# Performance work log

Measured on AMD Instinct MI355X. Metric: run time of the kernel, lower is better.

## Reference

```python
import jax, jax.numpy as jnp
import numpy as np
from jax import lax

N, D, K = 8192, 1024, 80
M = 2048            # pre-NMS candidate budget (jit-static stand-in for nonzero())
TOPK = 100
IMG_H, IMG_W = 800.0, 1216.0
BW = (10.0, 10.0, 5.0, 5.0)            # Box2BoxTransform weights
SCALE_CLAMP = float(np.log(1000.0 / 16.0))
SCORE_T, NMS_T = 0.05, 0.5
MAX_COORD = max(IMG_H, IMG_W) + 1.0    # class offset for batched NMS


def setup_inputs() -> dict:
    key = jax.random.key(0)
    ks = jax.random.split(key, 5)
    x = jax.random.normal(ks[0], (N, D), jnp.float32)
    cls_w = jax.random.normal(ks[1], (D, K + 1), jnp.float32) * 0.1
    cls_b = jnp.zeros((K + 1,), jnp.float32)
    bbox_w = jax.random.normal(ks[2], (D, K * 4), jnp.float32) * 0.001
    bbox_b = jnp.zeros((K * 4,), jnp.float32)
    xy = jax.random.uniform(ks[3], (N, 2)) * jnp.array([IMG_W * 0.8, IMG_H * 0.8])
    wh = jax.random.uniform(ks[4], (N, 2)) * jnp.array([IMG_W * 0.2, IMG_H * 0.2]) + 8.0
    proposals = jnp.concatenate([xy, xy + wh], axis=1).astype(jnp.float32)  # [N,4] xyxy
    return {"x": x, "cls_w": cls_w, "cls_b": cls_b,
            "bbox_w": bbox_w, "bbox_b": bbox_b, "proposals": proposals}


def _apply_deltas(deltas, boxes):
    # deltas [N,K,4], boxes [N,4] xyxy -> decoded [N,K,4]
    w = boxes[:, 2] - boxes[:, 0]
    h = boxes[:, 3] - boxes[:, 1]
    cx = boxes[:, 0] + 0.5 * w
    cy = boxes[:, 1] + 0.5 * h
    dx = deltas[..., 0] / BW[0]
    dy = deltas[..., 1] / BW[1]
    dw = jnp.minimum(deltas[..., 2] / BW[2], SCALE_CLAMP)
    dh = jnp.minimum(deltas[..., 3] / BW[3], SCALE_CLAMP)
    pcx = dx * w[:, None] + cx[:, None]
    pcy = dy * h[:, None] + cy[:, None]
    pw = jnp.exp(dw) * w[:, None]
    ph = jnp.exp(dh) * h[:, None]
    return jnp.stack([pcx - 0.5 * pw, pcy - 0.5 * ph,
                      pcx + 0.5 * pw, pcy + 0.5 * ph], axis=-1)


def _clip(b):
    x1 = jnp.clip(b[..., 0], 0.0, IMG_W)
    y1 = jnp.clip(b[..., 1], 0.0, IMG_H)
    x2 = jnp.clip(b[..., 2], 0.0, IMG_W)
    y2 = jnp.clip(b[..., 3], 0.0, IMG_H)
    return jnp.stack([x1, y1, x2, y2], axis=-1)


def _pairwise_iou(b):  # [M,4] -> [M,M]
    x1 = jnp.maximum(b[:, None, 0], b[None, :, 0])
    y1 = jnp.maximum(b[:, None, 1], b[None, :, 1])
    x2 = jnp.minimum(b[:, None, 2], b[None, :, 2])
    y2 = jnp.minimum(b[:, None, 3], b[None, :, 3])
    inter = jnp.maximum(x2 - x1, 0.0) * jnp.maximum(y2 - y1, 0.0)
    area = (b[:, 2] - b[:, 0]) * (b[:, 3] - b[:, 1])
    union = area[:, None] + area[None, :] - inter
    return inter / jnp.maximum(union, 1e-9)


def _pipeline(x, cls_w, cls_b, bbox_w, bbox_b, proposals):
    probs = jax.nn.softmax(x @ cls_w + cls_b, axis=-1)[:, :K]   # drop bg col
    deltas = (x @ bbox_w + bbox_b).reshape(N, K, 4)
    boxes = _clip(_apply_deltas(deltas, proposals))             # [N,K,4]

    flat = probs.reshape(-1)                                    # [N*K]
    cand = jnp.where(flat > SCORE_T, flat, -1.0)
    top_scores, top_idx = lax.top_k(cand, M)                    # sorted desc
    prop_idx = top_idx // K
    cls_idx = top_idx % K
    cand_boxes = boxes[prop_idx, cls_idx]                       # [M,4]
    valid = top_scores > SCORE_T

    # batched NMS via per-class coordinate offsets
    off = cls_idx.astype(cand_boxes.dtype)[:, None] * MAX_COORD
    iou = _pairwise_iou(cand_boxes + off)
    idxs = jnp.arange(M)

    def body(i, sup):
        alive = jnp.logical_and(~sup[i], valid[i])
        return sup | (alive & (iou[i] > NMS_T) & (idxs > i))

    sup = lax.fori_loop(0, M, body, jnp.zeros((M,), bool))
    keep = valid & ~sup

    kept_scores = jnp.where(keep, top_scores, -1.0)
    fscores, fidx = lax.top_k(kept_scores, TOPK)
    fboxes = cand_boxes[fidx]
    fcls = cls_idx[fidx]
    fvalid = keep[fidx]
    return fboxes, fscores, fcls, fvalid


def reference(x, cls_w, cls_b, bbox_w, bbox_b, proposals):
    return _pipeline(x, cls_w, cls_b, bbox_w, bbox_b, proposals)
```

## Files before the change

### kernel.cpp

```cpp
#include <hip/hip_runtime.h>
#include <math.h>

typedef unsigned long long u64;
typedef unsigned int u32;

#define N_ROWS 8192
#define DIM 1024
#define KCLS 80
#define KC1 81
#define MCAND 2048
#define TOPK_ 100
#define CMAX 65536
#define ECAP 4096
#define ROWS_CAP 4096
#define EROWS 3
#define EKS 4
#define EKL (DIM / EKS)
#define FRPB 8
#define NSPLIT 4
#define NBINS 8192
#define BIN_BASE 125440
#define LCAP 1024
#define SCORE_T 0.05
#define NMS_T 0.5f
#define MAX_COORD_F 1217.0f
#define SCALE_CLAMP_F 4.135166556742356f
#define IMG_W_F 1216.0f
#define IMG_H_F 800.0f

#define GBM 32
#define GBK 64
#define GKS 2
#define PSTR 96
#define WFRAG (32 * 6 * 64 * 8)

typedef __attribute__((ext_vector_type(8))) short bf16x8;
typedef __attribute__((ext_vector_type(4))) float f32x4;

__device__ __forceinline__ int score_bin_f(float p) {
  u32 bits = __float_as_uint(p);
  int b = (int)(bits >> 13) - BIN_BASE;
  return b < 0 ? 0 : (b > NBINS - 1 ? NBINS - 1 : b);
}

__device__ __forceinline__ u64 readlane64(u64 v, int l) {
  u32 lo = __builtin_amdgcn_readlane((u32)v, l);
  u32 hi = __builtin_amdgcn_readlane((u32)(v >> 32), l);
  return ((u64)hi << 32) | (u64)lo;
}

__device__ __forceinline__ ushort f32_bf16(float f) {
  u32 b = __float_as_uint(f);
  b += 0x7FFFu + ((b >> 16) & 1u);
  return (ushort)(b >> 16);
}

__global__ void k_init(int* counter, int* ecount, int* rowcnt, int* tbin,
                       int* hist, int* cnt, u32* rowflag,
                       double* selS, u32* selI) {
  int t = blockIdx.x * blockDim.x + threadIdx.x;
  if (t == 0) { *counter = 0; *ecount = 0; *rowcnt = 0; *tbin = 0; }
  if (t < NBINS) hist[t] = 0;
  if (t < N_ROWS) rowflag[t] = 0;
  if (t < ECAP) cnt[t] = 0;
  if (t < MCAND) { selS[t] = -1.0; selI[t] = 0u; }
}

__global__ __launch_bounds__(256) void k_bwt(const float4* __restrict__ bw4,
                                             float4* __restrict__ wT4) {
  int t = blockIdx.x * 256 + threadIdx.x;
  if (t < KCLS * DIM) {
    int k = t / KCLS;
    int cls = t - k * KCLS;
    wT4[(size_t)cls * DIM + k] = bw4[t];
  }
}

__global__ __launch_bounds__(256) void k_wprep(
    const float* __restrict__ w, ushort* __restrict__ whiF,
    ushort* __restrict__ wloF)
{
  int t = blockIdx.x * 256 + threadIdx.x;
  if (t >= WFRAG) return;
  int j = t & 7;
  int l = (t >> 3) & 63;
  int sf = t >> 9;
  int f = sf % 6;
  int s = sf / 6;
  int k = s * 32 + (l >> 4) * 8 + j;
  int c = f * 16 + (l & 15);
  float v = (c < KC1) ? w[(size_t)k * KC1 + c] : 0.0f;
  ushort hi = f32_bf16(v);
  float hf = __uint_as_float((u32)hi << 16);
  ushort lo = f32_bf16(v - hf);
  whiF[t] = hi;
  wloF[t] = lo;
}

__global__ __launch_bounds__(256) void k_gemm_mfma(
    const float* __restrict__ x, const ushort* __restrict__ whiF,
    const ushort* __restrict__ wloF, float* __restrict__ lgpart)
{
  __shared__ ushort xhi[GBM][72];
  __shared__ ushort xlo[GBM][72];
  __shared__ uint4 bhi[768];
  __shared__ uint4 blo[768];

  const int tid = threadIdx.x;
  const int rb = blockIdx.x * GBM;
  const int koff = blockIdx.y * (DIM / GKS);
  const int l = tid & 63;
  const int wv = tid >> 6;
  const int rh = wv & 1;
  const int ch = wv >> 1;

  f32x4 acc0 = {0.f, 0.f, 0.f, 0.f};
  f32x4 acc1 = {0.f, 0.f, 0.f, 0.f};
  f32x4 acc2 = {0.f, 0.f, 0.f, 0.f};

  const int srow = tid >> 3;
  const int skq = (tid & 7) * 8;
  const float* xsrc = x + (size_t)(rb + srow) * DIM + koff + skq;

  const int ar = rh * 16 + (l & 15);
  const int ak = (l >> 4) * 8;
  const int bbase = (ch * 3) * 64 + l;

  for (int kt = 0; kt < DIM / GKS; kt += GBK) {
    float4 xv0 = *(const float4*)(xsrc + kt);
    float4 xv1 = *(const float4*)(xsrc + kt + 4);
    const uint4* bh = (const uint4*)whiF + (size_t)((koff + kt) >> 5) * 384;
    const uint4* bl = (const uint4*)wloF + (size_t)((koff + kt) >> 5) * 384;
    uint4 h0 = bh[tid], h1 = bh[tid + 256], h2 = bh[tid + 512];
    uint4 g0 = bl[tid], g1 = bl[tid + 256], g2 = bl[tid + 512];

    __syncthreads();

    {
      float vv[8] = {xv0.x, xv0.y, xv0.z, xv0.w, xv1.x, xv1.y, xv1.z, xv1.w};
      u32 hw[4], lw[4];
#pragma unroll
      for (int q = 0; q < 4; ++q) {
        ushort ha = f32_bf16(vv[2 * q]);
        ushort hb = f32_bf16(vv[2 * q + 1]);
        ushort la = f32_bf16(vv[2 * q] - __uint_as_float((u32)ha << 16));
        ushort lb = f32_bf16(vv[2 * q + 1] - __uint_as_float((u32)hb << 16));
        hw[q] = (u32)ha | ((u32)hb << 16);
        lw[q] = (u32)la | ((u32)lb << 16);
      }
      *(uint4*)&xhi[srow][skq] = make_uint4(hw[0], hw[1], hw[2], hw[3]);
      *(uint4*)&xlo[srow][skq] = make_uint4(lw[0], lw[1], lw[2], lw[3]);
      bhi[tid] = h0; bhi[tid + 256] = h1; bhi[tid + 512] = h2;
      blo[tid] = g0; blo[tid + 256] = g1; blo[tid + 512] = g2;
    }
    __syncthreads();

#pragma unroll
    for (int ks = 0; ks < 2; ++ks) {
      bf16x8 ah = *(const bf16x8*)&xhi[ar][ks * 32 + ak];
      bf16x8 al = *(const bf16x8*)&xlo[ar][ks * 32 + ak];
      bf16x8 b0h = *(const bf16x8*)&bhi[ks * 384 + bbase];
      bf16x8 b0l = *(const bf16x8*)&blo[ks * 384 + bbase];
      bf16x8 b1h = *(const bf16x8*)&bhi[ks * 384 + bbase + 64];
      bf16x8 b1l = *(const bf16x8*)&blo[ks * 384 + bbase + 64];
      bf16x8 b2h = *(const bf16x8*)&bhi[ks * 384 + bbase + 128];
      bf16x8 b2l = *(const bf16x8*)&blo[ks * 384 + bbase + 128];
      acc0 = __builtin_amdgcn_mfma_f32_16x16x32_bf16(ah, b0h, acc0, 0, 0, 0);
      acc0 = __builtin_amdgcn_mfma_f32_16x16x32_bf16(ah, b0l, acc0, 0, 0, 0);
      acc0 = __builtin_amdgcn_mfma_f32_16x16x32_bf16(al, b0h, acc0, 0, 0, 0);
      acc1 = __builtin_amdgcn_mfma_f32_16x16x32_bf16(ah, b1h, acc1, 0, 0, 0);
      acc1 = __builtin_amdgcn_mfma_f32_16x16x32_bf16(ah, b1l, acc1, 0, 0, 0);
      acc1 = __builtin_amdgcn_mfma_f32_16x16x32_bf16(al, b1h, acc1, 0, 0, 0);
      acc2 = __builtin_amdgcn_mfma_f32_16x16x32_bf16(ah, b2h, acc2, 0, 0, 0);
      acc2 = __builtin_amdgcn_mfma_f32_16x16x32_bf16(ah, b2l, acc2, 0, 0, 0);
      acc2 = __builtin_amdgcn_mfma_f32_16x16x32_bf16(al, b2h, acc2, 0, 0, 0);
    }
  }

  float* dst = lgpart + (size_t)blockIdx.y * N_ROWS * PSTR;
  const int row0 = rb + rh * 16 + (l >> 4) * 4;
  const int col0 = ch * 48 + (l & 15);
#pragma unroll
  for (int r = 0; r < 4; ++r) {
    dst[(size_t)(row0 + r) * PSTR + col0 + 0]  = acc0[r];
    dst[(size_t)(row0 + r) * PSTR + col0 + 16] = acc1[r];
    dst[(size_t)(row0 + r) * PSTR + col0 + 32] = acc2[r];
  }
}

#define NE32P (32 * PSTR)
__global__ __launch_bounds__(256) void k_softmax32(
    const float* __restrict__ part, const float* __restrict__ bias,
    float* __restrict__ scf, u32* __restrict__ cid,
    int* __restrict__ counter, int* __restrict__ hist)
{
  __shared__ float lgs[NE32P];
  __shared__ float red[16][32];
  __shared__ float rowM[32];
  __shared__ float rowS[32];
  __shared__ u32 lhist[NBINS / 2];
  __shared__ float lscf[LCAP];
  __shared__ u32 lcid[LCAP];
  __shared__ int lcnt, gbase;
  const int tid = threadIdx.x;
  const int rb = blockIdx.x * 32;
  const int cx = tid >> 4;
  const int ry = tid & 15;

  if (tid == 0) lcnt = 0;
  for (int e = tid; e < NBINS / 2; e += 256) lhist[e] = 0u;

  {
    const float4* p0 = (const float4*)(part + ((size_t)0 * N_ROWS + rb) * PSTR);
    const float4* p1 = (const float4*)(part + ((size_t)1 * N_ROWS + rb) * PSTR);
    float4* dst = (float4*)lgs;
    for (int q = tid; q < NE32P / 4; q += 256) {
      float4 s0 = p0[q], s1 = p1[q];
      float4 t;
      t.x = s0.x + s1.x;
      t.y = s0.y + s1.y;
      t.z = s0.z + s1.z;
      t.w = s0.w + s1.w;
      dst[q] = t;
    }
  }
  __syncthreads();

  float lg[2][6];
#pragma unroll
  for (int i = 0; i < 2; i++) {
    int rloc = ry * 2 + i;
#pragma unroll
    for (int j = 0; j < 6; j++) {
      int c = cx * 6 + j;
      lg[i][j] = (c < KC1) ? (lgs[rloc * PSTR + c] + bias[c]) : -1e30f;
    }
  }
  float pm[2] = {-1e30f, -1e30f};
#pragma unroll
  for (int i = 0; i < 2; i++)
#pragma unroll
    for (int j = 0; j < 6; j++) pm[i] = fmaxf(pm[i], lg[i][j]);
  red[cx][ry * 2 + 0] = pm[0];
  red[cx][ry * 2 + 1] = pm[1];
  __syncthreads();
  if (tid < 32) {
    float m = -1e30f;
#pragma unroll
    for (int q = 0; q < 16; q++) m = fmaxf(m, red[q][tid]);
    rowM[tid] = m;
  }
  __syncthreads();
  float ps[2] = {0.0f, 0.0f};
#pragma unroll
  for (int i = 0; i < 2; i++) {
    float m = rowM[ry * 2 + i];
#pragma unroll
    for (int j = 0; j < 6; j++) {
      int c = cx * 6 + j;
      if (c < KC1) ps[i] += expf(lg[i][j] - m);
    }
  }
  __syncthreads();
  red[cx][ry * 2 + 0] = ps[0];
  red[cx][ry * 2 + 1] = ps[1];
  __syncthreads();
  if (tid < 32) {
    float s = 0.0f;
#pragma unroll
    for (int q = 0; q < 16; q++) s += red[q][tid];
    rowS[tid] = s;
  }
  __syncthreads();
#pragma unroll
  for (int i = 0; i < 2; i++) {
    int rloc = ry * 2 + i;
    float m = rowM[rloc], s = rowS[rloc];
#pragma unroll
    for (int j = 0; j < 6; j++) {
      int c = cx * 6 + j;
      if (c < KCLS) {
        float p = expf(lg[i][j] - m) / s;
        if (p > 0.0485f) {
          int pos = atomicAdd(&lcnt, 1);
          u32 idx = (u32)((rb + rloc) * KCLS + c);
          if (pos < LCAP) { lscf[pos] = p; lcid[pos] = idx; }
          else {
            int g = atomicAdd(counter, 1);
            if (g < CMAX) { scf[g] = p; cid[g] = idx; }
          }
        }
        if (p > 0.051f) {
          int b = score_bin_f(p);
          atomicAdd(&lhist[b >> 1], 1u << ((b & 1) * 16));
        }
      }
    }
  }
  __syncthreads();
  if (tid == 0) {
    int n = min(lcnt, LCAP);
    gbase = atomicAdd(counter, n);
  }
  __syncthreads();
  {
    int n = min(lcnt, LCAP);
    for (int e = tid; e < n; e += 256) {
      int g = gbase + e;
      if (g < CMAX) { scf[g] = lscf[e]; cid[g] = lcid[e]; }
    }
  }
  for (int q = tid; q < NBINS / 2; q += 256) {
    u32 v = lhist[q];
    if (v) {
      u32 lo = v & 0xFFFFu, hi = v >> 16;
      if (lo) atomicAdd(&hist[q * 2 + 0], (int)lo);
      if (hi) atomicAdd(&hist[q * 2 + 1], (int)hi);
    }
  }
}

__global__ __launch_bounds__(256) void k_thresh(
    const int* __restrict__ hist, int* __restrict__ tbin)
{
  __shared__ int h[NBINS];
  __shared__ int segsum[256];
  __shared__ int segsuf[256];
  const int tid = threadIdx.x;
  for (int e = tid; e < NBINS; e += 256) h[e] = hist[e];
  __syncthreads();
  int s = 0;
#pragma unroll
  for (int q = 0; q < NBINS / 256; ++q) s += h[tid * (NBINS / 256) + q];
  segsum[tid] = s;
  __syncthreads();
  if (tid == 0) {
    int run = 0;
    for (int t = 255; t >= 0; --t) { segsuf[t] = run; run += segsum[t]; }
  }
  __syncthreads();
  int run = segsuf[tid];
  if (run < MCAND) {
    const int lo = tid * (NBINS / 256);
    for (int b = lo + NBINS / 256 - 1; b >= lo; --b) {
      run += h[b];
      if (run >= MCAND) { *tbin = b; break; }
    }
  }
}

__global__ __launch_bounds__(256) void k_superset(
    const float* __restrict__ scf, const u32* __restrict__ cid,
    const int* __restrict__ counter, const int* __restrict__ tbin,
    u32* __restrict__ elist, int* __restrict__ ecount, u32* __restrict__ rowflag)
{
  int C = *counter; if (C > CMAX) C = CMAX;
  int TM = *tbin - 6; if (TM < 0) TM = 0;
  int e = blockIdx.x * 256 + threadIdx.x;
  const int lane = threadIdx.x & 63;
  bool pred = false;
  float p = 0.0f;
  if (e < C) {
    p = scf[e];
    pred = (score_bin_f(p) >= TM);
  }
  u64 m = __ballot(pred);
  if (m) {
    int leader = __ffsll((long long)m) - 1;
    int base = 0;
    if (lane == leader) base = atomicAdd(ecount, (int)__popcll(m));
    base = __shfl(base, leader);
    if (pred) {
      int j = base + (int)__popcll(m & ((lane == 63) ? ~0ull >> 1 : ((1ull << lane) - 1)));
      if (j < ECAP) {
        u32 idx = cid[e];
        elist[j] = idx;
        rowflag[idx / KCLS] = 1u;
      }
    }
  }
}

__global__ __launch_bounds__(256) void k_rowlist(
    const u32* __restrict__ rowflag, int* __restrict__ rowslot,
    u32* __restrict__ rowlist, int* __restrict__ rowcnt)
{
  int r = blockIdx.x * 256 + threadIdx.x;
  const int lane = threadIdx.x & 63;
  bool pred = (r < N_ROWS) && rowflag[r];
  u64 m = __ballot(pred);
  if (m) {
    int leader = __ffsll((long long)m) - 1;
    int base = 0;
    if (lane == leader) base = atomicAdd(rowcnt, (int)__popcll(m));
    base = __shfl(base, leader);
    if (pred) {
      int s = base + (int)__popcll(m & ((lane == 63) ? ~0ull >> 1 : ((1ull << lane) - 1)));
      if (s < ROWS_CAP) { rowslot[r] = s; rowlist[s] = (u32)r; }
    }
  }
}

__global__ __launch_bounds__(256) void k_exact_part(
    const u32* __restrict__ rowlist, const int* __restrict__ rowcnt,
    const float* __restrict__ x, const float* __restrict__ w,
    double* __restrict__ pexa)
{
  __shared__ double xt[EROWS][EKL];
  int rc = *rowcnt; if (rc > ROWS_CAP) rc = ROWS_CAP;
  const int rb = blockIdx.x * EROWS;
  if (rb >= rc) return;
  const int ks = blockIdx.y;
  const int kt0 = ks * EKL;
  const int tid = threadIdx.x;

  if (tid < EROWS * (EKL / 4)) {
    int srow = tid >> 6;
    int sf = tid & 63;
    int slot = rb + srow; if (slot >= rc) slot = rb;
    const float* xrow = x + (size_t)rowlist[slot] * DIM + kt0;
    float4 xv = *(const float4*)(xrow + sf * 4);
    xt[srow][sf * 4 + 0] = (double)xv.x;
    xt[srow][sf * 4 + 1] = (double)xv.y;
    xt[srow][sf * 4 + 2] = (double)xv.z;
    xt[srow][sf * 4 + 3] = (double)xv.w;
  }
  __syncthreads();

  const int row = tid / KC1;
  const int c = tid - row * KC1;
  if (row < EROWS && rb + row < rc) {
    const float* wp = w + (size_t)kt0 * KC1 + c;
    const double* xr = xt[row];
    double a = 0.0;
#pragma unroll 8
    for (int kk = 0; kk < EKL; ++kk) {
      a = fma(xr[kk], (double)wp[(size_t)kk * KC1], a);
    }
    pexa[((size_t)(rb + row) * EKS + ks) * KC1 + c] = a;
  }
}

__global__ __launch_bounds__(128) void k_exact_fin(
    const double* __restrict__ pexa, const int* __restrict__ rowcnt,
    const float* __restrict__ bias, double* __restrict__ prow)
{
  __shared__ double lg[FRPB][KC1];
  __shared__ double mv[FRPB], sv[FRPB];
  int rc = *rowcnt; if (rc > ROWS_CAP) rc = ROWS_CAP;
  const int rb = blockIdx.x * FRPB;
  if (rb >= rc) return;
  const int tid = threadIdx.x;
  const int nr = min(FRPB, rc - rb);

  if (tid < KC1) {
    for (int rr = 0; rr < nr; ++rr) {
      const double* pp = pexa + ((size_t)(rb + rr) * EKS) * KC1 + tid;
      double a = pp[0 * KC1];
      a += pp[1 * KC1];
      a += pp[2 * KC1];
      a += pp[3 * KC1];
      lg[rr][tid] = a + (double)bias[tid];
    }
  }
  __syncthreads();
  if (tid < nr) {
    double m = -1e300;
    for (int c2 = 0; c2 < KC1; ++c2) m = fmax(m, lg[tid][c2]);
    mv[tid] = m;
  }
  __syncthreads();
  if (tid < KC1) {
    for (int rr = 0; rr < nr; ++rr) lg[rr][tid] = exp(lg[rr][tid] - mv[rr]);
  }
  __syncthreads();
  if (tid < nr) {
    double s = 0.0;
    for (int c2 = 0; c2 < KC1; ++c2) s += lg[tid][c2];
    sv[tid] = s;
  }
  __syncthreads();
  if (tid < KC1) {
    for (int rr = 0; rr < nr; ++rr)
      prow[(size_t)(rb + rr) * KC1 + tid] = lg[rr][tid] / sv[rr];
  }
}

__global__ __launch_bounds__(256) void k_build(
    const u32* __restrict__ elist, const int* __restrict__ ecount,
    const int* __restrict__ rowslot, const double* __restrict__ prow,
    double* __restrict__ ssc, u32* __restrict__ sid)
{
  int E = *ecount; if (E > ECAP) E = ECAP;
  int e = blockIdx.x * 256 + threadIdx.x;
  if (e < E) {
    u32 idx = elist[e];
    int row = (int)(idx / KCLS);
    int cls = (int)(idx - (u32)row * KCLS);
    double p = prow[(size_t)rowslot[row] * KC1 + cls];
    ssc[e] = (p > SCORE_T) ? p : -1.0;
    sid[e] = idx;
  }
}

__global__ __launch_bounds__(256) void k_rank(
    const double* __restrict__ ssc, const u32* __restrict__ sid,
    const int* __restrict__ ecount, int* __restrict__ cnt)
{
  __shared__ double lsc[2048];
  __shared__ u32 lid[2048];
  int S = *ecount; if (S > ECAP) S = ECAP;
  const int i = blockIdx.x * 256 + threadIdx.x;
  if (blockIdx.x * 256 >= S) return;
  const double si = (i < S) ? ssc[i] : -2.0;
  const u32 ii = (i < S) ? sid[i] : 0u;
  const int seg = (S + NSPLIT - 1) / NSPLIT;
  const int jlo = blockIdx.y * seg;
  const int jhi = min(S, jlo + seg);
  int c = 0;
  for (int base = jlo; base < jhi; base += 2048) {
    const int n = min(2048, jhi - base);
    __syncthreads();
    for (int e = threadIdx.x; e < n; e += 256) { lsc[e] = ssc[base + e]; lid[e] = sid[base + e]; }
    __syncthreads();
    if (i < S) {
      for (int j = 0; j < n; ++j) {
        double sj = lsc[j];
        c += (sj > si || (sj == si && lid[j] < ii)) ? 1 : 0;
      }
    }
  }
  if (i < S && c > 0) atomicAdd(&cnt[i], c);
}

__global__ __launch_bounds__(256) void k_scatter(
    const double* __restrict__ ssc, const u32* __restrict__ sid,
    const int* __restrict__ ecount, const int* __restrict__ cnt,
    double* __restrict__ selS, u32* __restrict__ selI)
{
  int S = *ecount; if (S > ECAP) S = ECAP;
  const int i = blockIdx.x * 256 + threadIdx.x;
  if (i < S) {
    int c = cnt[i];
    if (c < MCAND) { selS[c] = ssc[i]; selI[c] = sid[i]; }
  }
}

__global__ __launch_bounds__(256) void k_gather_decode(
    const double* __restrict__ selS, const u32* __restrict__ selI,
    const float* __restrict__ x, const float4* __restrict__ wT4,
    const float* __restrict__ bbias, const float* __restrict__ proposals,
    float4* __restrict__ dbox, float4* __restrict__ obox,
    float* __restrict__ areav, float* __restrict__ scorev,
    int* __restrict__ clsv, int* __restrict__ validv)
{
  __shared__ double wred[4][4];
  const int r = blockIdx.x;
  const double s = selS[r];
  const u32 idx = selI[r];
  const int row = (int)(idx / 80u);
  const int cls = (int)(idx - (u32)row * 80u);

  const float* xr = x + (size_t)row * DIM;
  const float4* wc = wT4 + (size_t)cls * DIM;
  double a0 = 0, a1 = 0, a2 = 0, a3 = 0;
  for (int k = threadIdx.x; k < DIM; k += 256) {
    double xv = (double)xr[k];
    float4 wv = wc[k];
    a0 = fma(xv, (double)wv.x, a0);
    a1 = fma(xv, (double)wv.y, a1);
    a2 = fma(xv, (double)wv.z, a2);
    a3 = fma(xv, (double)wv.w, a3);
  }
#pragma unroll
  for (int off = 32; off > 0; off >>= 1) {
    a0 += __shfl_down(a0, off);
    a1 += __shfl_down(a1, off);
    a2 += __shfl_down(a2, off);
    a3 += __shfl_down(a3, off);
  }
  int lane = threadIdx.x & 63, wid = threadIdx.x >> 6;
  if (lane == 0) { wred[wid][0] = a0; wred[wid][1] = a1; wred[wid][2] = a2; wred[wid][3] = a3; }
  __syncthreads();
  if (threadIdx.x == 0) {
    double d0 = wred[0][0] + wred[1][0] + wred[2][0] + wred[3][0] + (double)bbias[cls * 4 + 0];
    double d1 = wred[0][1] + wred[1][1] + wred[2][1] + wred[3][1] + (double)bbias[cls * 4 + 1];
    double d2 = wred[0][2] + wred[1][2] + wred[2][2] + wred[3][2] + (double)bbias[cls * 4 + 2];
    double d3 = wred[0][3] + wred[1][3] + wred[2][3] + wred[3][3] + (double)bbias[cls * 4 + 3];
    float4 p = ((const float4*)proposals)[row];
    float w = p.z - p.x, h = p.w - p.y;
    float cxx = p.x + 0.5f * w, cyy = p.y + 0.5f * h;
    float dx = (float)d0 / 10.0f;
    float dy = (float)d1 / 10.0f;
    float dw = fminf((float)d2 / 5.0f, SCALE_CLAMP_F);
    float dh = fminf((float)d3 / 5.0f, SCALE_CLAMP_F);
    float pcx = dx * w + cxx, pcy = dy * h + cyy;
    float pw = expf(dw) * w, ph = expf(dh) * h;
    float x1 = pcx - 0.5f * pw, y1 = pcy - 0.5f * ph;
    float x2 = pcx + 0.5f * pw, y2 = pcy + 0.5f * ph;
    x1 = fminf(fmaxf(x1, 0.0f), IMG_W_F);
    x2 = fminf(fmaxf(x2, 0.0f), IMG_W_F);
    y1 = fminf(fmaxf(y1, 0.0f), IMG_H_F);
    y2 = fminf(fmaxf(y2, 0.0f), IMG_H_F);
    float4 db = {x1, y1, x2, y2};
    dbox[r] = db;
    float ofs = (float)cls * MAX_COORD_F;
    float4 ob = {x1 + ofs, y1 + ofs, x2 + ofs, y2 + ofs};
    obox[r] = ob;
    areav[r] = (ob.z - ob.x) * (ob.w - ob.y);
    scorev[r] = (float)s;
    clsv[r] = cls;
    validv[r] = (s > SCORE_T) ? 1 : 0;
  }
}

__global__ __launch_bounds__(256) void k_nms_mask(
    const float4* __restrict__ obox, const float* __restrict__ areav,
    u64* __restrict__ maskT)
{
  __shared__ float4 sb[MCAND];
  __shared__ float sa[MCAND];
  const int i = blockIdx.x;
  for (int e = threadIdx.x; e < MCAND; e += 256) { sb[e] = obox[e]; sa[e] = areav[e]; }
  __syncthreads();
  float4 bi = sb[i];
  float ai = sa[i];
  int lane = threadIdx.x & 63, wid = threadIdx.x >> 6;
#pragma unroll
  for (int it = 0; it < MCAND / 256; ++it) {
    int j = it * 256 + threadIdx.x;
    float4 bj = sb[j];
    float xx1 = fmaxf(bi.x, bj.x);
    float yy1 = fmaxf(bi.y, bj.y);
    float xx2 = fminf(bi.z, bj.z);
    float yy2 = fminf(bi.w, bj.w);
    float inter = fmaxf(xx2 - xx1, 0.0f) * fmaxf(yy2 - yy1, 0.0f);
    float uni = ai + sa[j] - inter;
    float iou = inter / fmaxf(uni, 1e-9f);
    bool pred = (iou > NMS_T) && (j > i);
    u64 b = __ballot(pred);
    if (lane == 0) maskT[(size_t)(it * 4 + wid) * MCAND + i] = b;
  }
}

__global__ __launch_bounds__(64) void k_nms_reduce(
    const u64* __restrict__ maskT, const int* __restrict__ validv,
    int* __restrict__ keep)
{
  const int lane = threadIdx.x;

  u64 validw = 0;
  for (int k = 0; k < 32; ++k) {
    u64 b = __ballot(validv[k * 64 + lane] != 0);
    validw = (lane == k) ? b : validw;
  }

  u64 alivew = 0;
  u64 supw = 0;
  int total = 0;
  int lastc = 31;

  for (int c = 0; c < 32; ++c) {
    const u64* col = maskT + (size_t)c * MCAND;
    u64 acc = 0;
    for (int t0 = 0; t0 < c; t0 += 8) {
      u64 r0 = 0, r1 = 0, r2 = 0, r3 = 0, r4 = 0, r5 = 0, r6 = 0, r7 = 0;
      if (t0 + 0 < c) r0 = col[(t0 + 0) * 64 + lane];
      if (t0 + 1 < c) r1 = col[(t0 + 1) * 64 + lane];
      if (t0 + 2 < c) r2 = col[(t0 + 2) * 64 + lane];
      if (t0 + 3 < c) r3 = col[(t0 + 3) * 64 + lane];
      if (t0 + 4 < c) r4 = col[(t0 + 4) * 64 + lane];
      if (t0 + 5 < c) r5 = col[(t0 + 5) * 64 + lane];
      if (t0 + 6 < c) r6 = col[(t0 + 6) * 64 + lane];
      if (t0 + 7 < c) r7 = col[(t0 + 7) * 64 + lane];
      u64 a;
      a = readlane64(alivew, t0 + 0); acc |= r0 & ((u64)0 - ((a >> lane) & 1ull));
      if (t0 + 1 < c) { a = readlane64(alivew, t0 + 1); acc |= r1 & ((u64)0 - ((a >> lane) & 1ull)); }
      if (t0 + 2 < c) { a = readlane64(alivew, t0 + 2); acc |= r2 & ((u64)0 - ((a >> lane) & 1ull)); }
      if (t0 + 3 < c) { a = readlane64(alivew, t0 + 3); acc |= r3 & ((u64)0 - ((a >> lane) & 1ull)); }
      if (t0 + 4 < c) { a = readlane64(alivew, t0 + 4); acc |= r4 & ((u64)0 - ((a >> lane) & 1ull)); }
      if (t0 + 5 < c) { a = readlane64(alivew, t0 + 5); acc |= r5 & ((u64)0 - ((a >> lane) & 1ull)); }
      if (t0 + 6 < c) { a = readlane64(alivew, t0 + 6); acc |= r6 & ((u64)0 - ((a >> lane) & 1ull)); }
      if (t0 + 7 < c) { a = readlane64(alivew, t0 + 7); acc |= r7 & ((u64)0 - ((a >> lane) & 1ull)); }
    }
    u64 d = col[(size_t)c * 64 + lane];
    acc |= (u64)__shfl_xor((long long)acc, 1);
    acc |= (u64)__shfl_xor((long long)acc, 2);
    acc |= (u64)__shfl_xor((long long)acc, 4);
    acc |= (u64)__shfl_xor((long long)acc, 8);
    acc |= (u64)__shfl_xor((long long)acc, 16);
    acc |= (u64)__shfl_xor((long long)acc, 32);
    u64 s_sup = acc;
    u64 s_val = readlane64(validw, c);
    u64 aliveM = 0;
#pragma unroll
    for (int b = 0; b < 64; ++b) {
      u32 rhi = __builtin_amdgcn_readlane((u32)(d >> 32), b);
      u32 rlo = (b < 31) ? __builtin_amdgcn_readlane((u32)d, b) : 0u;
      u64 row = ((u64)rhi << 32) | (u64)rlo;
      u64 act = ((s_val >> b) & 1ull) & (~(s_sup >> b) & 1ull);
      s_sup |= row & ((u64)0 - act);
      aliveM |= act << b;
    }
    alivew = (lane == c) ? aliveM : alivew;
    supw   = (lane == c) ? s_sup  : supw;
    total += (int)__popcll(aliveM);
    if (total >= TOPK_) { lastc = c; break; }
  }

  for (int k = 0; k < 32; ++k) {
    int e = k * 64 + lane;
    if (k <= lastc) {
      u64 s = readlane64(supw, k);
      int sb = (int)((s >> lane) & 1ull);
      keep[e] = (validv[e] && !sb) ? 1 : 0;
    } else {
      keep[e] = 0;
    }
  }
}

__global__ __launch_bounds__(256) void k_finalize(
    const int* __restrict__ keep, const float4* __restrict__ dbox,
    const float* __restrict__ scorev, const int* __restrict__ clsv,
    float* __restrict__ out)
{
  __shared__ short fidx[TOPK_];
  __shared__ char ksh[MCAND];
  const int tid = threadIdx.x;
  for (int e = tid; e < MCAND; e += 256) ksh[e] = (char)keep[e];
  __syncthreads();
  if (tid == 0) {
    int cnt = 0;
    for (int r = 0; r < MCAND && cnt < TOPK_; ++r) if (ksh[r]) fidx[cnt++] = (short)r;
    for (int r = 0; r < MCAND && cnt < TOPK_; ++r) if (!ksh[r]) fidx[cnt++] = (short)r;
  }
  __syncthreads();
  if (tid < TOPK_) {
    int r = fidx[tid];
    float4 b = dbox[r];
    out[tid * 4 + 0] = b.x; out[tid * 4 + 1] = b.y;
    out[tid * 4 + 2] = b.z; out[tid * 4 + 3] = b.w;
    int kp = ksh[r];
    out[400 + tid] = kp ? scorev[r] : -1.0f;
    out[500 + tid] = (float)clsv[r];
    out[600 + tid] = kp ? 1.0f : 0.0f;
  }
}

extern "C" void kernel_launch(void* const* d_in, const int* in_sizes, int n_in,
                              void* d_out, int out_size, void* d_ws, size_t ws_size,
                              hipStream_t stream) {
  const float* x         = (const float*)d_in[0];
  const float* cls_w     = (const float*)d_in[1];
  const float* cls_b     = (const float*)d_in[2];
  const float* bbox_w    = (const float*)d_in[3];
  const float* bbox_b    = (const float*)d_in[4];
  const float* proposals = (const float*)d_in[5];
  float* out = (float*)d_out;

  char* ws = (char*)d_ws;
  size_t off = 0;
  float*  part  = (float*)(ws + off);  off += (size_t)4 * N_ROWS * KC1 * 4;
  float4* wT4   = (float4*)(ws + off); off += (size_t)KCLS * DIM * 16;
  ushort* whiF  = (ushort*)(ws + off); off += (size_t)WFRAG * 2;
  ushort* wloF  = (ushort*)(ws + off); off += (size_t)WFRAG * 2;
  float*  scf   = (float*)(ws + off);  off += (size_t)CMAX * 4;
  u32*    cid   = (u32*)(ws + off);    off += (size_t)CMAX * 4;
  int*    hist  = (int*)(ws + off);    off += (size_t)NBINS * 4;
  u32*    rowflag = (u32*)(ws + off);  off += (size_t)N_ROWS * 4;
  int*    rowslot = (int*)(ws + off);  off += (size_t)N_ROWS * 4;
  u32*    rowlist = (u32*)(ws + off);  off += (size_t)ROWS_CAP * 4;
  u32*    elist = (u32*)(ws + off);    off += (size_t)ECAP * 4;
  double* prow  = (double*)(ws + off); off += (size_t)ROWS_CAP * KC1 * 8;
  double* ssc   = (double*)(ws + off); off += (size_t)ECAP * 8;
  u32*    sid   = (u32*)(ws + off);    off += (size_t)ECAP * 4;
  int*    cnt   = (int*)(ws + off);    off += (size_t)ECAP * 4;
  double* selS  = (double*)(ws + off); off += (size_t)MCAND * 8;
  u32*    selI  = (u32*)(ws + off);    off += (size_t)MCAND * 4;
  off = (off + 15) & ~(size_t)15;
  int*    counter = (int*)(ws + off);  off += 16;
  int*    ecount  = (int*)(ws + off);  off += 16;
  int*    rowcnt  = (int*)(ws + off);  off += 16;
  int*    tbin    = (int*)(ws + off);  off += 16;
  float4* dbox  = (float4*)(ws + off); off += (size_t)MCAND * 16;
  float4* obox  = (float4*)(ws + off); off += (size_t)MCAND * 16;
  float*  areav = (float*)(ws + off);  off += (size_t)MCAND * 4;
  float*  scorev= (float*)(ws + off);  off += (size_t)MCAND * 4;
  int*    clsv  = (int*)(ws + off);    off += (size_t)MCAND * 4;
  int*    validv= (int*)(ws + off);    off += (size_t)MCAND * 4;
  int*    keep  = (int*)(ws + off);    off += (size_t)MCAND * 4;
  off = (off + 15) & ~(size_t)15;
  u64*    maskT = (u64*)(ws + off);    off += (size_t)MCAND * 32 * 8;

  float* lgpart = part;
  double* pexa = (double*)part;

  k_init<<<N_ROWS / 256, 256, 0, stream>>>(counter, ecount, rowcnt, tbin, hist,
                                           cnt, rowflag, selS, selI);
  k_bwt<<<(KCLS * DIM + 255) / 256, 256, 0, stream>>>((const float4*)bbox_w, wT4);
  k_wprep<<<WFRAG / 256, 256, 0, stream>>>(cls_w, whiF, wloF);
  k_gemm_mfma<<<dim3(N_ROWS / GBM, GKS), 256, 0, stream>>>(x, whiF, wloF, lgpart);
  k_softmax32<<<N_ROWS / 32, 256, 0, stream>>>(lgpart, cls_b, scf, cid, counter, hist);
  k_thresh<<<1, 256, 0, stream>>>(hist, tbin);
  k_superset<<<CMAX / 256, 256, 0, stream>>>(scf, cid, counter, tbin, elist, ecount, rowflag);
  k_rowlist<<<N_ROWS / 256, 256, 0, stream>>>(rowflag, rowslot, rowlist, rowcnt);
  k_exact_part<<<dim3((ROWS_CAP + EROWS - 1) / EROWS, EKS), 256, 0, stream>>>(
      rowlist, rowcnt, x, cls_w, pexa);
  k_exact_fin<<<ROWS_CAP / FRPB, 128, 0, stream>>>(pexa, rowcnt, cls_b, prow);
  k_build<<<ECAP / 256, 256, 0, stream>>>(elist, ecount, rowslot, prow, ssc, sid);
  k_rank<<<dim3(ECAP / 256, NSPLIT), 256, 0, stream>>>(ssc, sid, ecount, cnt);
  k_scatter<<<ECAP / 256, 256, 0, stream>>>(ssc, sid, ecount, cnt, selS, selI);
  k_gather_decode<<<MCAND, 256, 0, stream>>>(selS, selI, x, wT4, bbox_b, proposals,
                                             dbox, obox, areav, scorev, clsv, validv);
  k_nms_mask<<<MCAND, 256, 0, stream>>>(obox, areav, maskT);
  k_nms_reduce<<<1, 64, 0, stream>>>(maskT, validv, keep);
  k_finalize<<<1, 256, 0, stream>>>(keep, dbox, scorev, clsv, out);
}
```

Before: 248.3 us.

## Fuse init/weight prep, GEMM+softmax, threshold+superset, and NMS reduce+finalize kernels

Merges init, bbox weight transpose and cls weight bf16 split into one prep kernel. Drops the split-K GEMM so each block computes full logits and runs the softmax/histogram epilogue from shared memory, removing the partial-logit round trip through global memory. Every superset block now recomputes the threshold bin from the histogram, and blocks past the candidate count exit early. NMS reduce and finalize are merged into one kernel using shared keep flags. The exchange is fewer launches and less global traffic against half as many GEMM blocks (256 instead of 512, less parallelism) and redundant per-block threshold scans.

```diff
diff --git a/kernel.cpp b/kernel.cpp
--- a/kernel.cpp
+++ b/kernel.cpp
@@ -30,7 +30,6 @@
 
 #define GBM 32
 #define GBK 64
-#define GKS 2
 #define PSTR 96
 #define WFRAG (32 * 6 * 64 * 8)
 
@@ -55,82 +54,87 @@
   return (ushort)(b >> 16);
 }
 
-__global__ void k_init(int* counter, int* ecount, int* rowcnt, int* tbin,
-                       int* hist, int* cnt, u32* rowflag,
-                       double* selS, u32* selI) {
-  int t = blockIdx.x * blockDim.x + threadIdx.x;
-  if (t == 0) { *counter = 0; *ecount = 0; *rowcnt = 0; *tbin = 0; }
+__global__ __launch_bounds__(256) void k_prep(
+    int* counter, int* ecount, int* rowcnt, int* hist, int* cnt,
+    u32* rowflag, double* selS, u32* selI,
+    const float4* __restrict__ bw4, float4* __restrict__ wT4,
+    const float* __restrict__ w, ushort* __restrict__ whiF,
+    ushort* __restrict__ wloF)
+{
+  int t = blockIdx.x * 256 + threadIdx.x;
+  if (t == 0) { *counter = 0; *ecount = 0; *rowcnt = 0; }
   if (t < NBINS) hist[t] = 0;
   if (t < N_ROWS) rowflag[t] = 0;
   if (t < ECAP) cnt[t] = 0;
   if (t < MCAND) { selS[t] = -1.0; selI[t] = 0u; }
-}
-
-__global__ __launch_bounds__(256) void k_bwt(const float4* __restrict__ bw4,
-                                             float4* __restrict__ wT4) {
-  int t = blockIdx.x * 256 + threadIdx.x;
   if (t < KCLS * DIM) {
     int k = t / KCLS;
     int cls = t - k * KCLS;
     wT4[(size_t)cls * DIM + k] = bw4[t];
   }
-}
-
-__global__ __launch_bounds__(256) void k_wprep(
-    const float* __restrict__ w, ushort* __restrict__ whiF,
-    ushort* __restrict__ wloF)
-{
-  int t = blockIdx.x * 256 + threadIdx.x;
-  if (t >= WFRAG) return;
-  int j = t & 7;
-  int l = (t >> 3) & 63;
-  int sf = t >> 9;
-  int f = sf % 6;
-  int s = sf / 6;
-  int k = s * 32 + (l >> 4) * 8 + j;
-  int c = f * 16 + (l & 15);
-  float v = (c < KC1) ? w[(size_t)k * KC1 + c] : 0.0f;
-  ushort hi = f32_bf16(v);
-  float hf = __uint_as_float((u32)hi << 16);
-  ushort lo = f32_bf16(v - hf);
-  whiF[t] = hi;
-  wloF[t] = lo;
-}
-
-__global__ __launch_bounds__(256) void k_gemm_mfma(
+  if (t < WFRAG) {
+    int j = t & 7;
+    int l = (t >> 3) & 63;
+    int sf = t >> 9;
+    int f = sf % 6;
+    int s = sf / 6;
+    int k = s * 32 + (l >> 4) * 8 + j;
+    int c = f * 16 + (l & 15);
+    float v = (c < KC1) ? w[(size_t)k * KC1 + c] : 0.0f;
+    ushort hi = f32_bf16(v);
+    float hf = __uint_as_float((u32)hi << 16);
+    whiF[t] = hi;
+    wloF[t] = f32_bf16(v - hf);
+  }
+}
+
+__global__ __launch_bounds__(256) void k_gemm_sm(
     const float* __restrict__ x, const ushort* __restrict__ whiF,
-    const ushort* __restrict__ wloF, float* __restrict__ lgpart)
-{
-  __shared__ ushort xhi[GBM][72];
-  __shared__ ushort xlo[GBM][72];
-  __shared__ uint4 bhi[768];
-  __shared__ uint4 blo[768];
+    const ushort* __restrict__ wloF, const float* __restrict__ bias,
+    float* __restrict__ scf, u32* __restrict__ cid,
+    int* __restrict__ counter, int* __restrict__ hist)
+{
+  __shared__ __align__(16) char smem[33792];
+  __shared__ float lgs[GBM * PSTR];
+  __shared__ int lcnt, gbase;
+
+  ushort (*xhi)[72] = (ushort(*)[72])(smem);
+  ushort (*xlo)[72] = (ushort(*)[72])(smem + 4608);
+  uint4* bhi = (uint4*)(smem + 9216);
+  uint4* blo = (uint4*)(smem + 21504);
+  u32* lhist = (u32*)(smem);
+  float* lscf = (float*)(smem + 16384);
+  u32* lcid = (u32*)(smem + 20480);
+  float (*red)[32] = (float(*)[32])(smem + 24576);
+  float* rowM = (float*)(smem + 26624);
+  float* rowS = (float*)(smem + 26752);
 
   const int tid = threadIdx.x;
   const int rb = blockIdx.x * GBM;
-  const int koff = blockIdx.y * (DIM / GKS);
   const int l = tid & 63;
   const int wv = tid >> 6;
   const int rh = wv & 1;
   const int ch = wv >> 1;
 
+  if (tid == 0) lcnt = 0;
+
   f32x4 acc0 = {0.f, 0.f, 0.f, 0.f};
   f32x4 acc1 = {0.f, 0.f, 0.f, 0.f};
   f32x4 acc2 = {0.f, 0.f, 0.f, 0.f};
 
   const int srow = tid >> 3;
   const int skq = (tid & 7) * 8;
-  const float* xsrc = x + (size_t)(rb + srow) * DIM + koff + skq;
+  const float* xsrc = x + (size_t)(rb + srow) * DIM + skq;
 
   const int ar = rh * 16 + (l & 15);
   const int ak = (l >> 4) * 8;
   const int bbase = (ch * 3) * 64 + l;
 
-  for (int kt = 0; kt < DIM / GKS; kt += GBK) {
+  for (int kt = 0; kt < DIM; kt += GBK) {
     float4 xv0 = *(const float4*)(xsrc + kt);
     float4 xv1 = *(const float4*)(xsrc + kt + 4);
-    const uint4* bh = (const uint4*)whiF + (size_t)((koff + kt) >> 5) * 384;
-    const uint4* bl = (const uint4*)wloF + (size_t)((koff + kt) >> 5) * 384;
+    const uint4* bh = (const uint4*)whiF + (size_t)(kt >> 5) * 384;
+    const uint4* bl = (const uint4*)wloF + (size_t)(kt >> 5) * 384;
     uint4 h0 = bh[tid], h1 = bh[tid + 256], h2 = bh[tid + 512];
     uint4 g0 = bl[tid], g1 = bl[tid + 256], g2 = bl[tid + 512];
 
@@ -177,55 +181,22 @@
     }
   }
 
-  float* dst = lgpart + (size_t)blockIdx.y * N_ROWS * PSTR;
-  const int row0 = rb + rh * 16 + (l >> 4) * 4;
-  const int col0 = ch * 48 + (l & 15);
-#pragma unroll
-  for (int r = 0; r < 4; ++r) {
-    dst[(size_t)(row0 + r) * PSTR + col0 + 0]  = acc0[r];
-    dst[(size_t)(row0 + r) * PSTR + col0 + 16] = acc1[r];
-    dst[(size_t)(row0 + r) * PSTR + col0 + 32] = acc2[r];
-  }
-}
-
-#define NE32P (32 * PSTR)
-__global__ __launch_bounds__(256) void k_softmax32(
-    const float* __restrict__ part, const float* __restrict__ bias,
-    float* __restrict__ scf, u32* __restrict__ cid,
-    int* __restrict__ counter, int* __restrict__ hist)
-{
-  __shared__ float lgs[NE32P];
-  __shared__ float red[16][32];
-  __shared__ float rowM[32];
-  __shared__ float rowS[32];
-  __shared__ u32 lhist[NBINS / 2];
-  __shared__ float lscf[LCAP];
-  __shared__ u32 lcid[LCAP];
-  __shared__ int lcnt, gbase;
-  const int tid = threadIdx.x;
-  const int rb = blockIdx.x * 32;
+  __syncthreads();
+  {
+    const int row0l = rh * 16 + (l >> 4) * 4;
+    const int col0 = ch * 48 + (l & 15);
+#pragma unroll
+    for (int r = 0; r < 4; ++r) {
+      lgs[(row0l + r) * PSTR + col0 + 0]  = acc0[r];
+      lgs[(row0l + r) * PSTR + col0 + 16] = acc1[r];
+      lgs[(row0l + r) * PSTR + col0 + 32] = acc2[r];
+    }
+  }
+  for (int e = tid; e < NBINS / 2; e += 256) lhist[e] = 0u;
+  __syncthreads();
+
   const int cx = tid >> 4;
   const int ry = tid & 15;
-
-  if (tid == 0) lcnt = 0;
-  for (int e = tid; e < NBINS / 2; e += 256) lhist[e] = 0u;
-
-  {
-    const float4* p0 = (const float4*)(part + ((size_t)0 * N_ROWS + rb) * PSTR);
-    const float4* p1 = (const float4*)(part + ((size_t)1 * N_ROWS + rb) * PSTR);
-    float4* dst = (float4*)lgs;
-    for (int q = tid; q < NE32P / 4; q += 256) {
-      float4 s0 = p0[q], s1 = p1[q];
-      float4 t;
-      t.x = s0.x + s1.x;
-      t.y = s0.y + s1.y;
-      t.z = s0.z + s1.z;
-      t.w = s0.w + s1.w;
-      dst[q] = t;
-    }
-  }
-  __syncthreads();
-
   float lg[2][6];
 #pragma unroll
   for (int i = 0; i < 2; i++) {
@@ -320,50 +291,49 @@
   }
 }
 
-__global__ __launch_bounds__(256) void k_thresh(
-    const int* __restrict__ hist, int* __restrict__ tbin)
+__global__ __launch_bounds__(256) void k_superset(
+    const float* __restrict__ scf, const u32* __restrict__ cid,
+    const int* __restrict__ counter, const int* __restrict__ hist,
+    u32* __restrict__ elist, int* __restrict__ ecount, u32* __restrict__ rowflag)
 {
   __shared__ int h[NBINS];
   __shared__ int segsum[256];
   __shared__ int segsuf[256];
+  __shared__ int tbin_s;
+  int C = *counter; if (C > CMAX) C = CMAX;
+  if (blockIdx.x * 256 >= C) return;
   const int tid = threadIdx.x;
+  if (tid == 0) tbin_s = 0;
   for (int e = tid; e < NBINS; e += 256) h[e] = hist[e];
   __syncthreads();
-  int s = 0;
-#pragma unroll
-  for (int q = 0; q < NBINS / 256; ++q) s += h[tid * (NBINS / 256) + q];
-  segsum[tid] = s;
+  {
+    int s = 0;
+#pragma unroll
+    for (int q = 0; q < NBINS / 256; ++q) s += h[tid * (NBINS / 256) + q];
+    segsum[tid] = s;
+  }
   __syncthreads();
   if (tid == 0) {
     int run = 0;
     for (int t = 255; t >= 0; --t) { segsuf[t] = run; run += segsum[t]; }
   }
   __syncthreads();
-  int run = segsuf[tid];
-  if (run < MCAND) {
-    const int lo = tid * (NBINS / 256);
-    for (int b = lo + NBINS / 256 - 1; b >= lo; --b) {
-      run += h[b];
-      if (run >= MCAND) { *tbin = b; break; }
-    }
-  }
-}
-
-__global__ __launch_bounds__(256) void k_superset(
-    const float* __restrict__ scf, const u32* __restrict__ cid,
-    const int* __restrict__ counter, const int* __restrict__ tbin,
-    u32* __restrict__ elist, int* __restrict__ ecount, u32* __restrict__ rowflag)
-{
-  int C = *counter; if (C > CMAX) C = CMAX;
-  int TM = *tbin - 6; if (TM < 0) TM = 0;
-  int e = blockIdx.x * 256 + threadIdx.x;
-  const int lane = threadIdx.x & 63;
+  {
+    int run = segsuf[tid];
+    if (run < MCAND) {
+      const int lo = tid * (NBINS / 256);
+      for (int b = lo + NBINS / 256 - 1; b >= lo; --b) {
+        run += h[b];
+        if (run >= MCAND) { tbin_s = b; break; }
+      }
+    }
+  }
+  __syncthreads();
+  int TM = tbin_s - 6; if (TM < 0) TM = 0;
+  int e = blockIdx.x * 256 + tid;
+  const int lane = tid & 63;
   bool pred = false;
-  float p = 0.0f;
-  if (e < C) {
-    p = scf[e];
-    pred = (score_bin_f(p) >= TM);
-  }
+  if (e < C) pred = (score_bin_f(scf[e]) >= TM);
   u64 m = __ballot(pred);
   if (m) {
     int leader = __ffsll((long long)m) - 1;
@@ -643,92 +613,87 @@
   }
 }
 
-__global__ __launch_bounds__(64) void k_nms_reduce(
+__global__ __launch_bounds__(256) void k_nms_fin(
     const u64* __restrict__ maskT, const int* __restrict__ validv,
-    int* __restrict__ keep)
-{
-  const int lane = threadIdx.x;
-
-  u64 validw = 0;
-  for (int k = 0; k < 32; ++k) {
-    u64 b = __ballot(validv[k * 64 + lane] != 0);
-    validw = (lane == k) ? b : validw;
-  }
-
-  u64 alivew = 0;
-  u64 supw = 0;
-  int total = 0;
-  int lastc = 31;
-
-  for (int c = 0; c < 32; ++c) {
-    const u64* col = maskT + (size_t)c * MCAND;
-    u64 acc = 0;
-    for (int t0 = 0; t0 < c; t0 += 8) {
-      u64 r0 = 0, r1 = 0, r2 = 0, r3 = 0, r4 = 0, r5 = 0, r6 = 0, r7 = 0;
-      if (t0 + 0 < c) r0 = col[(t0 + 0) * 64 + lane];
-      if (t0 + 1 < c) r1 = col[(t0 + 1) * 64 + lane];
-      if (t0 + 2 < c) r2 = col[(t0 + 2) * 64 + lane];
-      if (t0 + 3 < c) r3 = col[(t0 + 3) * 64 + lane];
-      if (t0 + 4 < c) r4 = col[(t0 + 4) * 64 + lane];
-      if (t0 + 5 < c) r5 = col[(t0 + 5) * 64 + lane];
-      if (t0 + 6 < c) r6 = col[(t0 + 6) * 64 + lane];
-      if (t0 + 7 < c) r7 = col[(t0 + 7) * 64 + lane];
-      u64 a;
-      a = readlane64(alivew, t0 + 0); acc |= r0 & ((u64)0 - ((a >> lane) & 1ull));
-      if (t0 + 1 < c) { a = readlane64(alivew, t0 + 1); acc |= r1 & ((u64)0 - ((a >> lane) & 1ull)); }
-      if (t0 + 2 < c) { a = readlane64(alivew, t0 + 2); acc |= r2 & ((u64)0 - ((a >> lane) & 1ull)); }
-      if (t0 + 3 < c) { a = readlane64(alivew, t0 + 3); acc |= r3 & ((u64)0 - ((a >> lane) & 1ull)); }
-      if (t0 + 4 < c) { a = readlane64(alivew, t0 + 4); acc |= r4 & ((u64)0 - ((a >> lane) & 1ull)); }
-      if (t0 + 5 < c) { a = readlane64(alivew, t0 + 5); acc |= r5 & ((u64)0 - ((a >> lane) & 1ull)); }
-      if (t0 + 6 < c) { a = readlane64(alivew, t0 + 6); acc |= r6 & ((u64)0 - ((a >> lane) & 1ull)); }
-      if (t0 + 7 < c) { a = readlane64(alivew, t0 + 7); acc |= r7 & ((u64)0 - ((a >> lane) & 1ull)); }
-    }
-    u64 d = col[(size_t)c * 64 + lane];
-    acc |= (u64)__shfl_xor((long long)acc, 1);
-    acc |= (u64)__shfl_xor((long long)acc, 2);
-    acc |= (u64)__shfl_xor((long long)acc, 4);
-    acc |= (u64)__shfl_xor((long long)acc, 8);
-    acc |= (u64)__shfl_xor((long long)acc, 16);
-    acc |= (u64)__shfl_xor((long long)acc, 32);
-    u64 s_sup = acc;
-    u64 s_val = readlane64(validw, c);
-    u64 aliveM = 0;
-#pragma unroll
-    for (int b = 0; b < 64; ++b) {
-      u32 rhi = __builtin_amdgcn_readlane((u32)(d >> 32), b);
-      u32 rlo = (b < 31) ? __builtin_amdgcn_readlane((u32)d, b) : 0u;
-      u64 row = ((u64)rhi << 32) | (u64)rlo;
-      u64 act = ((s_val >> b) & 1ull) & (~(s_sup >> b) & 1ull);
-      s_sup |= row & ((u64)0 - act);
-      aliveM |= act << b;
-    }
-    alivew = (lane == c) ? aliveM : alivew;
-    supw   = (lane == c) ? s_sup  : supw;
-    total += (int)__popcll(aliveM);
-    if (total >= TOPK_) { lastc = c; break; }
-  }
-
-  for (int k = 0; k < 32; ++k) {
-    int e = k * 64 + lane;
-    if (k <= lastc) {
-      u64 s = readlane64(supw, k);
-      int sb = (int)((s >> lane) & 1ull);
-      keep[e] = (validv[e] && !sb) ? 1 : 0;
-    } else {
-      keep[e] = 0;
-    }
-  }
-}
-
-__global__ __launch_bounds__(256) void k_finalize(
-    const int* __restrict__ keep, const float4* __restrict__ dbox,
-    const float* __restrict__ scorev, const int* __restrict__ clsv,
-    float* __restrict__ out)
-{
+    const float4* __restrict__ dbox, const float* __restrict__ scorev,
+    const int* __restrict__ clsv, float* __restrict__ out)
+{
+  __shared__ char ksh[MCAND];
   __shared__ short fidx[TOPK_];
-  __shared__ char ksh[MCAND];
   const int tid = threadIdx.x;
-  for (int e = tid; e < MCAND; e += 256) ksh[e] = (char)keep[e];
+
+  if (tid < 64) {
+    const int lane = tid;
+    u64 validw = 0;
+    for (int k = 0; k < 32; ++k) {
+      u64 b = __ballot(validv[k * 64 + lane] != 0);
+      validw = (lane == k) ? b : validw;
+    }
+
+    u64 alivew = 0;
+    u64 supw = 0;
+    int total = 0;
+    int lastc = 31;
+
+    for (int c = 0; c < 32; ++c) {
+      const u64* col = maskT + (size_t)c * MCAND;
+      u64 acc = 0;
+      for (int t0 = 0; t0 < c; t0 += 8) {
+        u64 r0 = 0, r1 = 0, r2 = 0, r3 = 0, r4 = 0, r5 = 0, r6 = 0, r7 = 0;
+        if (t0 + 0 < c) r0 = col[(t0 + 0) * 64 + lane];
+        if (t0 + 1 < c) r1 = col[(t0 + 1) * 64 + lane];
+        if (t0 + 2 < c) r2 = col[(t0 + 2) * 64 + lane];
+        if (t0 + 3 < c) r3 = col[(t0 + 3) * 64 + lane];
+        if (t0 + 4 < c) r4 = col[(t0 + 4) * 64 + lane];
+        if (t0 + 5 < c) r5 = col[(t0 + 5) * 64 + lane];
+        if (t0 + 6 < c) r6 = col[(t0 + 6) * 64 + lane];
+        if (t0 + 7 < c) r7 = col[(t0 + 7) * 64 + lane];
+        u64 a;
+        a = readlane64(alivew, t0 + 0); acc |= r0 & ((u64)0 - ((a >> lane) & 1ull));
+        if (t0 + 1 < c) { a = readlane64(alivew, t0 + 1); acc |= r1 & ((u64)0 - ((a >> lane) & 1ull)); }
+        if (t0 + 2 < c) { a = readlane64(alivew, t0 + 2); acc |= r2 & ((u64)0 - ((a >> lane) & 1ull)); }
+        if (t0 + 3 < c) { a = readlane64(alivew, t0 + 3); acc |= r3 & ((u64)0 - ((a >> lane) & 1ull)); }
+        if (t0 + 4 < c) { a = readlane64(alivew, t0 + 4); acc |= r4 & ((u64)0 - ((a >> lane) & 1ull)); }
+        if (t0 + 5 < c) { a = readlane64(alivew, t0 + 5); acc |= r5 & ((u64)0 - ((a >> lane) & 1ull)); }
+        if (t0 + 6 < c) { a = readlane64(alivew, t0 + 6); acc |= r6 & ((u64)0 - ((a >> lane) & 1ull)); }
+        if (t0 + 7 < c) { a = readlane64(alivew, t0 + 7); acc |= r7 & ((u64)0 - ((a >> lane) & 1ull)); }
+      }
+      u64 d = col[(size_t)c * 64 + lane];
+      acc |= (u64)__shfl_xor((long long)acc, 1);
+      acc |= (u64)__shfl_xor((long long)acc, 2);
+      acc |= (u64)__shfl_xor((long long)acc, 4);
+      acc |= (u64)__shfl_xor((long long)acc, 8);
+      acc |= (u64)__shfl_xor((long long)acc, 16);
+      acc |= (u64)__shfl_xor((long long)acc, 32);
+      u64 s_sup = acc;
+      u64 s_val = readlane64(validw, c);
+      u64 aliveM = 0;
+#pragma unroll
+      for (int b = 0; b < 64; ++b) {
+        u32 rhi = __builtin_amdgcn_readlane((u32)(d >> 32), b);
+        u32 rlo = (b < 31) ? __builtin_amdgcn_readlane((u32)d, b) : 0u;
+        u64 row = ((u64)rhi << 32) | (u64)rlo;
+        u64 act = ((s_val >> b) & 1ull) & (~(s_sup >> b) & 1ull);
+        s_sup |= row & ((u64)0 - act);
+        aliveM |= act << b;
+      }
+      alivew = (lane == c) ? aliveM : alivew;
+      supw   = (lane == c) ? s_sup  : supw;
+      total += (int)__popcll(aliveM);
+      if (total >= TOPK_) { lastc = c; break; }
+    }
+
+    for (int k = 0; k < 32; ++k) {
+      int e = k * 64 + lane;
+      if (k <= lastc) {
+        u64 s = readlane64(supw, k);
+        int sb = (int)((s >> lane) & 1ull);
+        ksh[e] = (char)((validv[e] && !sb) ? 1 : 0);
+      } else {
+        ksh[e] = 0;
+      }
+    }
+  }
   __syncthreads();
   if (tid == 0) {
     int cnt = 0;
@@ -782,28 +747,25 @@
   int*    counter = (int*)(ws + off);  off += 16;
   int*    ecount  = (int*)(ws + off);  off += 16;
   int*    rowcnt  = (int*)(ws + off);  off += 16;
-  int*    tbin    = (int*)(ws + off);  off += 16;
   float4* dbox  = (float4*)(ws + off); off += (size_t)MCAND * 16;
   float4* obox  = (float4*)(ws + off); off += (size_t)MCAND * 16;
   float*  areav = (float*)(ws + off);  off += (size_t)MCAND * 4;
   float*  scorev= (float*)(ws + off);  off += (size_t)MCAND * 4;
   int*    clsv  = (int*)(ws + off);    off += (size_t)MCAND * 4;
   int*    validv= (int*)(ws + off);    off += (size_t)MCAND * 4;
-  int*    keep  = (int*)(ws + off);    off += (size_t)MCAND * 4;
   off = (off + 15) & ~(size_t)15;
   u64*    maskT = (u64*)(ws + off);    off += (size_t)MCAND * 32 * 8;
 
-  float* lgpart = part;
   double* pexa = (double*)part;
 
-  k_init<<<N_ROWS / 256, 256, 0, stream>>>(counter, ecount, rowcnt, tbin, hist,
-                                           cnt, rowflag, selS, selI);
-  k_bwt<<<(KCLS * DIM + 255) / 256, 256, 0, stream>>>((const float4*)bbox_w, wT4);
-  k_wprep<<<WFRAG / 256, 256, 0, stream>>>(cls_w, whiF, wloF);
-  k_gemm_mfma<<<dim3(N_ROWS / GBM, GKS), 256, 0, stream>>>(x, whiF, wloF, lgpart);
-  k_softmax32<<<N_ROWS / 32, 256, 0, stream>>>(lgpart, cls_b, scf, cid, counter, hist);
-  k_thresh<<<1, 256, 0, stream>>>(hist, tbin);
-  k_superset<<<CMAX / 256, 256, 0, stream>>>(scf, cid, counter, tbin, elist, ecount, rowflag);
+  k_prep<<<WFRAG / 256, 256, 0, stream>>>(counter, ecount, rowcnt, hist, cnt,
+                                          rowflag, selS, selI,
+                                          (const float4*)bbox_w, wT4,
+                                          cls_w, whiF, wloF);
+  k_gemm_sm<<<N_ROWS / GBM, 256, 0, stream>>>(x, whiF, wloF, cls_b,
+                                              scf, cid, counter, hist);
+  k_superset<<<CMAX / 256, 256, 0, stream>>>(scf, cid, counter, hist,
+                                             elist, ecount, rowflag);
   k_rowlist<<<N_ROWS / 256, 256, 0, stream>>>(rowflag, rowslot, rowlist, rowcnt);
   k_exact_part<<<dim3((ROWS_CAP + EROWS - 1) / EROWS, EKS), 256, 0, stream>>>(
       rowlist, rowcnt, x, cls_w, pexa);
@@ -814,6 +776,5 @@
   k_gather_decode<<<MCAND, 256, 0, stream>>>(selS, selI, x, wT4, bbox_b, proposals,
                                              dbox, obox, areav, scorev, clsv, validv);
   k_nms_mask<<<MCAND, 256, 0, stream>>>(obox, areav, maskT);
-  k_nms_reduce<<<1, 64, 0, stream>>>(maskT, validv, keep);
-  k_finalize<<<1, 256, 0, stream>>>(keep, dbox, scorev, clsv, out);
-}
+  k_nms_fin<<<1, 256, 0, stream>>>(maskT, validv, dbox, scorev, clsv, out);
+}
```

Measured after the change: 244.3 us. About the same (-1.6%).
